# Performance work log

Hardware: AMD Instinct MI355X
Metric: run time of the kernel (lower is better)

Reference implementation:

```python
import jax, jax.numpy as jnp
import numpy as np

T, H, E, K, G, TG, F, NSH = 1024, 1024, 64, 6, 8, 4, 512, 2
CAP = 384
SCALE = 2.5  # routed_scaling_factor


def setup_inputs() -> dict:
    key = jax.random.key(0)
    ks = jax.random.split(key, 7)
    return {
        'hidden_states': jax.random.normal(ks[0], (T, H), jnp.float32),
        'gate_w': jax.random.normal(ks[1], (E, H), jnp.float32) * 0.05,
        'bias': jax.random.normal(ks[2], (E,), jnp.float32) * 0.01,
        'w13': jax.random.normal(ks[3], (E, H, 2 * F), jnp.float32) * 0.02,
        'w2': jax.random.normal(ks[4], (E, F, H), jnp.float32) * 0.02,
        'sw13': jax.random.normal(ks[5], (H, 2 * F * NSH), jnp.float32) * 0.02,
        'sw2': jax.random.normal(ks[6], (F * NSH, H), jnp.float32) * 0.02,
    }


def _grouped_topk(logits, bias):
    # noaux_tc: sigmoid scores, bias-corrected group selection, weights from raw scores
    scores = jax.nn.sigmoid(logits)                      # [T,E]
    sc = scores + bias[None, :]
    grp = sc.reshape(-1, G, E // G)
    group_scores = jnp.sum(jax.lax.top_k(grp, 2)[0], -1)  # [T,G] sum of top-2 per group
    _, gidx = jax.lax.top_k(group_scores, TG)
    gmask = jnp.sum(jax.nn.one_hot(gidx, G, dtype=sc.dtype), axis=1)  # [T,G]
    emask = jnp.repeat(gmask, E // G, axis=1) > 0
    masked = jnp.where(emask, sc, -jnp.inf)
    _, topk_ids = jax.lax.top_k(masked, K)               # [T,K]
    w = jnp.take_along_axis(scores, topk_ids, axis=1)
    w = w / jnp.sum(w, -1, keepdims=True) * SCALE        # renormalize + scaling
    return w, topk_ids


def reference(hidden_states, gate_w, bias, w13, w2, sw13, sw2):
    x = hidden_states
    # shared experts MLP (SiluAndMul)
    gu_s = x @ sw13
    shared = (jax.nn.silu(gu_s[:, :F * NSH]) * gu_s[:, F * NSH:]) @ sw2

    # gate in fp32
    logits = x.astype(jnp.float32) @ gate_w.T
    topk_w, topk_ids = _grouped_topk(logits, bias)

    # dispatch to [E, CAP, H]
    flat = topk_ids.reshape(-1)                           # [T*K]
    oh = (flat[:, None] == jnp.arange(E)[None, :])
    pos = jnp.sum(jnp.cumsum(oh.astype(jnp.int32), 0) * oh, 1) - 1  # rank within expert
    slot = jnp.minimum(pos, CAP)
    x_rep = jnp.broadcast_to(x[:, None, :], (T, K, H)).reshape(-1, H)
    buf = jnp.zeros((E, CAP + 1, H), x.dtype).at[flat, slot].set(x_rep)[:, :CAP]

    # grouped expert MLP
    gu = jnp.einsum('ech,ehf->ecf', buf, w13)             # [E,CAP,2F]
    act = jax.nn.silu(gu[..., :F]) * gu[..., F:]
    eo = jnp.einsum('ecf,efh->ech', act, w2)              # [E,CAP,H]

    # combine
    valid = (pos < CAP).astype(x.dtype)[:, None]
    yk = eo[flat, jnp.minimum(pos, CAP - 1)] * valid      # [T*K,H]
    routed = jnp.sum(yk.reshape(T, K, H) * topk_w[..., None].astype(x.dtype), axis=1)
    return routed + shared
```

## Files before the change

kernel.cpp:

```cpp
#include <hip/hip_runtime.h>
#include <cstdint>

#define TT   1024
#define HH   1024
#define EE   64
#define KK   6
#define GG   8
#define TGn  4
#define FF   512
#define FN   1024
#define CAPc 384
#define SCALEs 2.5f

typedef unsigned int u32;
typedef unsigned short u16;
typedef short short8 __attribute__((ext_vector_type(8)));
typedef float f32x4 __attribute__((ext_vector_type(4)));
union ABu { uint4 u; short8 s; };

__device__ __forceinline__ u32 pack_bf16(float a, float b) {
  u32 ua = __float_as_uint(a) + 0x8000u;
  u32 ub = __float_as_uint(b) + 0x8000u;
  return __builtin_amdgcn_perm(ub, ua, 0x07060302u);
}
__device__ __forceinline__ u16 bf16_1(float a) {
  return (u16)((__float_as_uint(a) + 0x8000u) >> 16);
}
__device__ __forceinline__ float bf2f(u32 lo16) {
  return __uint_as_float(lo16 << 16);
}

__global__ __launch_bounds__(256) void convert_x(const float* __restrict__ x,
                                                 u32* __restrict__ xb) {
  const int i = blockIdx.x * 256 + threadIdx.x;
  float4 v = ((const float4*)x)[i];
  uint2 o;
  o.x = pack_bf16(v.x, v.y);
  o.y = pack_bf16(v.z, v.w);
  ((uint2*)xb)[i] = o;
}

__global__ __launch_bounds__(256) void gate_topk_kernel(
    const float* __restrict__ x, const float* __restrict__ gw,
    const float* __restrict__ bias, int* __restrict__ ids,
    float* __restrict__ tw) {
  __shared__ float xs[HH];
  __shared__ float part[256];
  __shared__ float sc[EE];
  __shared__ float scores[EE];
  const int t = blockIdx.x, tid = threadIdx.x;
  ((float4*)xs)[tid] = ((const float4*)(x + (size_t)t * HH))[tid];
  __syncthreads();
  {
    const int e = tid & 63, seg = tid >> 6;
    const float* w = gw + (size_t)e * HH + seg * 256;
    const float* xv = xs + seg * 256;
    float acc = 0.f;
#pragma unroll 8
    for (int i = 0; i < 256; ++i) acc = fmaf(xv[i], w[i], acc);
    part[tid] = acc;
  }
  __syncthreads();
  if (tid < 64) {
    float a = part[tid] + part[tid + 64] + part[tid + 128] + part[tid + 192];
    float s = 1.f / (1.f + expf(-a));
    scores[tid] = s;
    sc[tid] = s + bias[tid];
  }
  __syncthreads();
  if (tid == 0) {
    float gs[GG];
    for (int g = 0; g < GG; ++g) {
      float m1 = -1e30f, m2 = -1e30f;
      for (int j = 0; j < EE / GG; ++j) {
        float v = sc[g * (EE / GG) + j];
        if (v > m1) { m2 = m1; m1 = v; }
        else if (v > m2) { m2 = v; }
      }
      gs[g] = m1 + m2;
    }
    unsigned gmask = 0;
    for (int r = 0; r < TGn; ++r) {
      int best = -1; float bv = -1e30f;
      for (int g = 0; g < GG; ++g)
        if (!((gmask >> g) & 1u) && gs[g] > bv) { bv = gs[g]; best = g; }
      gmask |= 1u << best;
    }
    unsigned long long used = 0ull;
    float wsum = 0.f;
    int idbuf[KK]; float wbuf[KK];
    for (int r = 0; r < KK; ++r) {
      int best = -1; float bv = -3e38f;
      for (int e = 0; e < EE; ++e) {
        if (!((gmask >> (e / (EE / GG))) & 1u)) continue;
        if ((used >> e) & 1ull) continue;
        float v = sc[e];
        if (v > bv) { bv = v; best = e; }
      }
      used |= 1ull << best;
      idbuf[r] = best;
      wbuf[r] = scores[best];
      wsum += scores[best];
    }
    const float inv = SCALEs / wsum;
    for (int r = 0; r < KK; ++r) {
      ids[t * KK + r] = idbuf[r];
      tw[t * KK + r] = wbuf[r] * inv;
    }
  }
}

__global__ void dispatch_kernel(const int* __restrict__ ids,
                                int* __restrict__ counts,
                                int* __restrict__ tok_of,
                                int* __restrict__ slot_of) {
  const int i = blockIdx.x * blockDim.x + threadIdx.x;
  if (i >= TT * KK) return;
  const int e = ids[i];
  const int p = atomicAdd(&counts[e], 1);
  slot_of[i] = p;
  if (p < CAPc) tok_of[e * CAPc + p] = i / KK;
}

#define SA 20
#define SB 132

template<int MT, int FH, bool ROUTED>
__global__ __launch_bounds__(256) void gemm1_k(
    const u32* __restrict__ xb, const float* __restrict__ wsrc,
    const int* __restrict__ counts, const int* __restrict__ tok_of,
    u16* __restrict__ actp) {
  constexpr int WROW = 2 * FH;
  constexpr int RT = MT / 32;
  constexpr int ADW = MT * 16 / 256;
  const int e = ROUTED ? blockIdx.z : 0;
  int n_e = MT;
  if (ROUTED) {
    n_e = min(counts[e], CAPc);
    if ((int)(blockIdx.y * MT) >= n_e) return;
  }
  const int m0 = blockIdx.y * MT;
  const int n0 = blockIdx.x * 64;
  __shared__ __align__(16) u32 As[MT * SA];
  __shared__ __align__(16) u32 Bs[16 * SB];
  __shared__ int toks[MT];
  const int tid = threadIdx.x;
  if (ROUTED) {
    for (int i = tid; i < MT; i += 256)
      toks[i] = (m0 + i < n_e) ? tok_of[e * CAPc + m0 + i] : -1;
    __syncthreads();
  }
  const int wave = tid >> 6, lane = tid & 63, quad = lane >> 4, l16 = lane & 15;
  const int ww = wave & 1, wr = wave >> 1;
  const float* W = wsrc + (ROUTED ? (size_t)e * HH * WROW : 0);
  const int arow_i = tid & (MT - 1);
  const int akd = (MT == 128 ? (tid >> 7) : (tid >> 6)) * ADW;
  bool aok = true;
  const u32* arow;
  if (ROUTED) {
    int tk = toks[arow_i];
    aok = tk >= 0;
    arow = xb + (size_t)(aok ? tk : 0) * (HH / 2);
  } else {
    arow = xb + (size_t)(m0 + arow_i) * (HH / 2);
  }
  const int bkd0 = tid >> 5, bn4 = (tid & 31) << 2;
  const int bcol = (bn4 < 64) ? (n0 + bn4) : (FH + n0 + (bn4 - 64));

  uint4 apf[ADW / 4];
  float4 bpf[2][2];
  auto prefetch = [&](int k0) {
#pragma unroll
    for (int i = 0; i < ADW / 4; ++i) {
      uint4 v = *(const uint4*)(arow + (k0 >> 1) + akd + 4 * i);
      if (!aok) v = make_uint4(0u, 0u, 0u, 0u);
      apf[i] = v;
    }
#pragma unroll
    for (int i = 0; i < 2; ++i) {
      const float* p = W + (size_t)(k0 + 2 * (bkd0 + 8 * i)) * WROW + bcol;
      bpf[i][0] = *(const float4*)p;
      bpf[i][1] = *(const float4*)(p + WROW);
    }
  };
  prefetch(0);
  f32x4 acc[RT][4] = {};
  for (int k0 = 0; k0 < HH; k0 += 32) {
    __syncthreads();
#pragma unroll
    for (int i = 0; i < ADW / 4; ++i)
      *(uint4*)(&As[arow_i * SA + akd + 4 * i]) = apf[i];
#pragma unroll
    for (int i = 0; i < 2; ++i) {
      uint4 bv;
      bv.x = pack_bf16(bpf[i][0].x, bpf[i][1].x);
      bv.y = pack_bf16(bpf[i][0].y, bpf[i][1].y);
      bv.z = pack_bf16(bpf[i][0].z, bpf[i][1].z);
      bv.w = pack_bf16(bpf[i][0].w, bpf[i][1].w);
      *(uint4*)(&Bs[(bkd0 + 8 * i) * SB + bn4]) = bv;
    }
    __syncthreads();
    if (k0 + 32 < HH) prefetch(k0 + 32);
    ABu bfr[4];
#pragma unroll
    for (int j = 0; j < 4; ++j) {
      const int cb = (j < 2) ? (ww * 32 + j * 16) : (64 + ww * 32 + (j - 2) * 16);
      const int col = cb + l16;
      bfr[j].u.x = Bs[(quad * 4 + 0) * SB + col];
      bfr[j].u.y = Bs[(quad * 4 + 1) * SB + col];
      bfr[j].u.z = Bs[(quad * 4 + 2) * SB + col];
      bfr[j].u.w = Bs[(quad * 4 + 3) * SB + col];
    }
#pragma unroll
    for (int mi = 0; mi < RT; ++mi) {
      ABu a;
      a.u = *(const uint4*)(&As[(wr * (MT / 2) + mi * 16 + l16) * SA + quad * 4]);
#pragma unroll
      for (int j = 0; j < 4; ++j)
        acc[mi][j] = __builtin_amdgcn_mfma_f32_16x16x32_bf16(a.s, bfr[j].s, acc[mi][j], 0, 0, 0);
    }
  }
#pragma unroll
  for (int mi = 0; mi < RT; ++mi) {
#pragma unroll
    for (int j = 0; j < 2; ++j) {
      const int col = n0 + ww * 32 + j * 16 + l16;
#pragma unroll
      for (int r = 0; r < 4; ++r) {
        const int row = m0 + wr * (MT / 2) + mi * 16 + quad * 4 + r;
        const float g = acc[mi][j][r], u = acc[mi][j + 2][r];
        const float v = (g / (1.f + __expf(-g))) * u;
        size_t idx = ROUTED ? (((size_t)e * CAPc + row) * FH + col)
                            : ((size_t)row * FH + col);
        actp[idx] = bf16_1(v);
      }
    }
  }
}

template<int MT, int KD, bool ROUTED>
__global__ __launch_bounds__(256) void gemm2_k(
    const u32* __restrict__ asrc0, const float* __restrict__ wsrc,
    const int* __restrict__ counts, void* __restrict__ outp) {
  constexpr int RT = MT / 32;
  constexpr int ADW = MT * 16 / 256;
  const int e = ROUTED ? blockIdx.z : 0;
  if (ROUTED) {
    if ((int)(blockIdx.y * MT) >= min(counts[e], CAPc)) return;
  }
  const int m0 = blockIdx.y * MT;
  const int n0 = blockIdx.x * 128;
  __shared__ __align__(16) u32 As[MT * SA];
  __shared__ __align__(16) u32 Bs[16 * SB];
  const int tid = threadIdx.x;
  const int wave = tid >> 6, lane = tid & 63, quad = lane >> 4, l16 = lane & 15;
  const int ww = wave & 1, wr = wave >> 1;
  const float* W = wsrc + (ROUTED ? (size_t)e * KD * HH : 0);
  const int arow_i = tid & (MT - 1);
  const int akd = (MT == 128 ? (tid >> 7) : (tid >> 6)) * ADW;
  const u32* arow = asrc0 + (ROUTED ? ((size_t)e * CAPc + m0 + arow_i) * (KD / 2)
                                    : (size_t)(m0 + arow_i) * (KD / 2));
  const int bkd0 = tid >> 5, bn4 = (tid & 31) << 2;

  uint4 apf[ADW / 4];
  float4 bpf[2][2];
  auto prefetch = [&](int k0) {
#pragma unroll
    for (int i = 0; i < ADW / 4; ++i)
      apf[i] = *(const uint4*)(arow + (k0 >> 1) + akd + 4 * i);
#pragma unroll
    for (int i = 0; i < 2; ++i) {
      const float* p = W + (size_t)(k0 + 2 * (bkd0 + 8 * i)) * HH + n0 + bn4;
      bpf[i][0] = *(const float4*)p;
      bpf[i][1] = *(const float4*)(p + HH);
    }
  };
  prefetch(0);
  f32x4 acc[RT][4] = {};
  for (int k0 = 0; k0 < KD; k0 += 32) {
    __syncthreads();
#pragma unroll
    for (int i = 0; i < ADW / 4; ++i)
      *(uint4*)(&As[arow_i * SA + akd + 4 * i]) = apf[i];
#pragma unroll
    for (int i = 0; i < 2; ++i) {
      uint4 bv;
      bv.x = pack_bf16(bpf[i][0].x, bpf[i][1].x);
      bv.y = pack_bf16(bpf[i][0].y, bpf[i][1].y);
      bv.z = pack_bf16(bpf[i][0].z, bpf[i][1].z);
      bv.w = pack_bf16(bpf[i][0].w, bpf[i][1].w);
      *(uint4*)(&Bs[(bkd0 + 8 * i) * SB + bn4]) = bv;
    }
    __syncthreads();
    if (k0 + 32 < KD) prefetch(k0 + 32);
    ABu bfr[4];
#pragma unroll
    for (int j = 0; j < 4; ++j) {
      const int col = ww * 64 + j * 16 + l16;
      bfr[j].u.x = Bs[(quad * 4 + 0) * SB + col];
      bfr[j].u.y = Bs[(quad * 4 + 1) * SB + col];
      bfr[j].u.z = Bs[(quad * 4 + 2) * SB + col];
      bfr[j].u.w = Bs[(quad * 4 + 3) * SB + col];
    }
#pragma unroll
    for (int mi = 0; mi < RT; ++mi) {
      ABu a;
      a.u = *(const uint4*)(&As[(wr * (MT / 2) + mi * 16 + l16) * SA + quad * 4]);
#pragma unroll
      for (int j = 0; j < 4; ++j)
        acc[mi][j] = __builtin_amdgcn_mfma_f32_16x16x32_bf16(a.s, bfr[j].s, acc[mi][j], 0, 0, 0);
    }
  }
#pragma unroll
  for (int mi = 0; mi < RT; ++mi) {
#pragma unroll
    for (int j = 0; j < 4; ++j) {
      const int col = n0 + ww * 64 + j * 16 + l16;
#pragma unroll
      for (int r = 0; r < 4; ++r) {
        const int row = m0 + wr * (MT / 2) + mi * 16 + quad * 4 + r;
        if (ROUTED) {
          ((u16*)outp)[((size_t)e * CAPc + row) * HH + col] = bf16_1(acc[mi][j][r]);
        } else {
          ((float*)outp)[(size_t)row * HH + col] = acc[mi][j][r];
        }
      }
    }
  }
}

__global__ __launch_bounds__(256) void combine_k(
    const u16* __restrict__ eo, const int* __restrict__ ids,
    const int* __restrict__ slot_of, const float* __restrict__ tw,
    float* __restrict__ out) {
  const int t = blockIdx.x, tid = threadIdx.x;
  __shared__ int se[KK];
  __shared__ int ssl[KK];
  __shared__ float swt[KK];
  if (tid < KK) {
    se[tid] = ids[t * KK + tid];
    ssl[tid] = slot_of[t * KK + tid];
    swt[tid] = tw[t * KK + tid];
  }
  __syncthreads();
  const int h = tid * 4;
  float4 o = *(float4*)(&out[(size_t)t * HH + h]);
#pragma unroll
  for (int k = 0; k < KK; ++k) {
    if (ssl[k] >= CAPc) continue;
    const float wgt = swt[k];
    const u16* p = eo + ((size_t)se[k] * CAPc + ssl[k]) * HH + h;
    uint2 v = *(const uint2*)p;
    o.x = fmaf(wgt, bf2f(v.x & 0xffffu), o.x);
    o.y = fmaf(wgt, bf2f(v.x >> 16), o.y);
    o.z = fmaf(wgt, bf2f(v.y & 0xffffu), o.z);
    o.w = fmaf(wgt, bf2f(v.y >> 16), o.w);
  }
  *(float4*)(&out[(size_t)t * HH + h]) = o;
}

extern "C" void kernel_launch(void* const* d_in, const int* in_sizes, int n_in,
                              void* d_out, int out_size, void* d_ws, size_t ws_size,
                              hipStream_t stream) {
  const float* x    = (const float*)d_in[0];
  const float* gw   = (const float*)d_in[1];
  const float* bias = (const float*)d_in[2];
  const float* w13  = (const float*)d_in[3];
  const float* w2   = (const float*)d_in[4];
  const float* sw13 = (const float*)d_in[5];
  const float* sw2  = (const float*)d_in[6];
  float* out = (float*)d_out;

  char* ws = (char*)d_ws;
  size_t off = 0;
  int*   counts  = (int*)(ws + off);   off += 256;
  int*   tok_of  = (int*)(ws + off);   off += (size_t)EE * CAPc * 4;
  int*   ids     = (int*)(ws + off);   off += (size_t)TT * KK * 4;
  int*   slot_of = (int*)(ws + off);   off += (size_t)TT * KK * 4;
  float* tw      = (float*)(ws + off); off += (size_t)TT * KK * 4;
  off = (off + 255) & ~(size_t)255;
  u32*   xb      = (u32*)(ws + off);   off += (size_t)TT * HH * 2;
  u16*   act     = (u16*)(ws + off);   off += (size_t)EE * CAPc * FF * 2;
  u16*   eo      = (u16*)(ws + off);   off += (size_t)EE * CAPc * HH * 2;
  u16*   act_s   = (u16*)(ws + off);   off += (size_t)TT * FN * 2;

  hipMemsetAsync(counts, 0, 256, stream);
  convert_x<<<TT * HH / 1024, 256, 0, stream>>>(x, xb);
  gate_topk_kernel<<<TT, 256, 0, stream>>>(x, gw, bias, ids, tw);
  dispatch_kernel<<<(TT * KK + 255) / 256, 256, 0, stream>>>(ids, counts, tok_of, slot_of);
  gemm1_k<128, FF, true><<<dim3(FF / 64, CAPc / 128, EE), 256, 0, stream>>>(
      xb, w13, counts, tok_of, act);
  gemm2_k<128, FF, true><<<dim3(HH / 128, CAPc / 128, EE), 256, 0, stream>>>(
      (const u32*)act, w2, counts, eo);
  gemm1_k<64, FN, false><<<dim3(FN / 64, TT / 64), 256, 0, stream>>>(
      xb, sw13, nullptr, nullptr, act_s);
  gemm2_k<64, FN, false><<<dim3(HH / 128, TT / 64), 256, 0, stream>>>(
      (const u32*)act_s, sw2, nullptr, out);
  combine_k<<<TT, 256, 0, stream>>>(eo, ids, slot_of, tw, out);
}
```

Before: 633.0 us.

## Fuse gate/convert/dispatch, double-buffer GEMM prefetch, narrow shared gemm2 tile

Merges the bf16 conversion of x, the gate/top-k, and the dispatch atomics into one kernel, removing two launches. The GEMM kernels now prefetch two k-steps ahead using double-buffered registers, to hide global-load latency. The shared-expert down-projection uses a 64-wide N tile, doubling its block count for better occupancy. Register pressure rises from the extra prefetch buffers.

```diff
diff --git a/kernel.cpp b/kernel.cpp
--- a/kernel.cpp
+++ b/kernel.cpp
@@ -30,26 +30,22 @@
   return __uint_as_float(lo16 << 16);
 }
 
-__global__ __launch_bounds__(256) void convert_x(const float* __restrict__ x,
-                                                 u32* __restrict__ xb) {
-  const int i = blockIdx.x * 256 + threadIdx.x;
-  float4 v = ((const float4*)x)[i];
-  uint2 o;
-  o.x = pack_bf16(v.x, v.y);
-  o.y = pack_bf16(v.z, v.w);
-  ((uint2*)xb)[i] = o;
-}
-
-__global__ __launch_bounds__(256) void gate_topk_kernel(
+__global__ __launch_bounds__(256) void gate_fused(
     const float* __restrict__ x, const float* __restrict__ gw,
-    const float* __restrict__ bias, int* __restrict__ ids,
-    float* __restrict__ tw) {
+    const float* __restrict__ bias, u32* __restrict__ xb,
+    int* __restrict__ counts, int* __restrict__ tok_of,
+    int* __restrict__ ids, int* __restrict__ slot_of, float* __restrict__ tw) {
   __shared__ float xs[HH];
   __shared__ float part[256];
   __shared__ float sc[EE];
   __shared__ float scores[EE];
   const int t = blockIdx.x, tid = threadIdx.x;
-  ((float4*)xs)[tid] = ((const float4*)(x + (size_t)t * HH))[tid];
+  float4 v = ((const float4*)(x + (size_t)t * HH))[tid];
+  ((float4*)xs)[tid] = v;
+  uint2 o;
+  o.x = pack_bf16(v.x, v.y);
+  o.y = pack_bf16(v.z, v.w);
+  ((uint2*)xb)[t * (HH / 4) + tid] = o;
   __syncthreads();
   {
     const int e = tid & 63, seg = tid >> 6;
@@ -73,9 +69,9 @@
     for (int g = 0; g < GG; ++g) {
       float m1 = -1e30f, m2 = -1e30f;
       for (int j = 0; j < EE / GG; ++j) {
-        float v = sc[g * (EE / GG) + j];
-        if (v > m1) { m2 = m1; m1 = v; }
-        else if (v > m2) { m2 = v; }
+        float v2 = sc[g * (EE / GG) + j];
+        if (v2 > m1) { m2 = m1; m1 = v2; }
+        else if (v2 > m2) { m2 = v2; }
       }
       gs[g] = m1 + m2;
     }
@@ -94,8 +90,8 @@
       for (int e = 0; e < EE; ++e) {
         if (!((gmask >> (e / (EE / GG))) & 1u)) continue;
         if ((used >> e) & 1ull) continue;
-        float v = sc[e];
-        if (v > bv) { bv = v; best = e; }
+        float v2 = sc[e];
+        if (v2 > bv) { bv = v2; best = e; }
       }
       used |= 1ull << best;
       idbuf[r] = best;
@@ -104,26 +100,19 @@
     }
     const float inv = SCALEs / wsum;
     for (int r = 0; r < KK; ++r) {
-      ids[t * KK + r] = idbuf[r];
+      const int e = idbuf[r];
+      const int p = atomicAdd(&counts[e], 1);
+      if (p < CAPc) tok_of[e * CAPc + p] = t;
+      ids[t * KK + r] = e;
+      slot_of[t * KK + r] = p;
       tw[t * KK + r] = wbuf[r] * inv;
     }
   }
-}
-
-__global__ void dispatch_kernel(const int* __restrict__ ids,
-                                int* __restrict__ counts,
-                                int* __restrict__ tok_of,
-                                int* __restrict__ slot_of) {
-  const int i = blockIdx.x * blockDim.x + threadIdx.x;
-  if (i >= TT * KK) return;
-  const int e = ids[i];
-  const int p = atomicAdd(&counts[e], 1);
-  slot_of[i] = p;
-  if (p < CAPc) tok_of[e * CAPc + p] = i / KK;
 }
 
 #define SA 20
 #define SB 132
+#define SB2 68
 
 template<int MT, int FH, bool ROUTED>
 __global__ __launch_bounds__(256) void gemm1_k(
@@ -133,6 +122,7 @@
   constexpr int WROW = 2 * FH;
   constexpr int RT = MT / 32;
   constexpr int ADW = MT * 16 / 256;
+  constexpr int AV = ADW / 4;
   const int e = ROUTED ? blockIdx.z : 0;
   int n_e = MT;
   if (ROUTED) {
@@ -167,40 +157,42 @@
   const int bkd0 = tid >> 5, bn4 = (tid & 31) << 2;
   const int bcol = (bn4 < 64) ? (n0 + bn4) : (FH + n0 + (bn4 - 64));
 
-  uint4 apf[ADW / 4];
-  float4 bpf[2][2];
-  auto prefetch = [&](int k0) {
-#pragma unroll
-    for (int i = 0; i < ADW / 4; ++i) {
+  uint4 apf[2][AV];
+  float4 bpf[2][2][2];
+  auto prefetch = [&](int k0, int p) {
+#pragma unroll
+    for (int i = 0; i < AV; ++i) {
       uint4 v = *(const uint4*)(arow + (k0 >> 1) + akd + 4 * i);
       if (!aok) v = make_uint4(0u, 0u, 0u, 0u);
-      apf[i] = v;
+      apf[p][i] = v;
     }
 #pragma unroll
     for (int i = 0; i < 2; ++i) {
-      const float* p = W + (size_t)(k0 + 2 * (bkd0 + 8 * i)) * WROW + bcol;
-      bpf[i][0] = *(const float4*)p;
-      bpf[i][1] = *(const float4*)(p + WROW);
+      const float* ptr = W + (size_t)(k0 + 2 * (bkd0 + 8 * i)) * WROW + bcol;
+      bpf[p][i][0] = *(const float4*)ptr;
+      bpf[p][i][1] = *(const float4*)(ptr + WROW);
     }
   };
-  prefetch(0);
+  prefetch(0, 0);
+  prefetch(32, 1);
   f32x4 acc[RT][4] = {};
   for (int k0 = 0; k0 < HH; k0 += 32) {
-    __syncthreads();
-#pragma unroll
-    for (int i = 0; i < ADW / 4; ++i)
-      *(uint4*)(&As[arow_i * SA + akd + 4 * i]) = apf[i];
+    const int p = (k0 >> 5) & 1;
+    __syncthreads();
+#pragma unroll
+    for (int i = 0; i < AV; ++i)
+      *(uint4*)(&As[arow_i * SA + akd + 4 * i]) = apf[p][i];
 #pragma unroll
     for (int i = 0; i < 2; ++i) {
       uint4 bv;
-      bv.x = pack_bf16(bpf[i][0].x, bpf[i][1].x);
-      bv.y = pack_bf16(bpf[i][0].y, bpf[i][1].y);
-      bv.z = pack_bf16(bpf[i][0].z, bpf[i][1].z);
-      bv.w = pack_bf16(bpf[i][0].w, bpf[i][1].w);
+      bv.x = pack_bf16(bpf[p][i][0].x, bpf[p][i][1].x);
+      bv.y = pack_bf16(bpf[p][i][0].y, bpf[p][i][1].y);
+      bv.z = pack_bf16(bpf[p][i][0].z, bpf[p][i][1].z);
+      bv.w = pack_bf16(bpf[p][i][0].w, bpf[p][i][1].w);
       *(uint4*)(&Bs[(bkd0 + 8 * i) * SB + bn4]) = bv;
     }
     __syncthreads();
-    if (k0 + 32 < HH) prefetch(k0 + 32);
+    if (k0 + 64 < HH) prefetch(k0 + 64, p);
     ABu bfr[4];
 #pragma unroll
     for (int j = 0; j < 4; ++j) {
@@ -238,20 +230,23 @@
   }
 }
 
-template<int MT, int KD, bool ROUTED>
+template<int MT, int NT, int KD, bool ROUTED>
 __global__ __launch_bounds__(256) void gemm2_k(
     const u32* __restrict__ asrc0, const float* __restrict__ wsrc,
     const int* __restrict__ counts, void* __restrict__ outp) {
   constexpr int RT = MT / 32;
+  constexpr int CT = NT / 32;
   constexpr int ADW = MT * 16 / 256;
+  constexpr int AV = ADW / 4;
+  constexpr int SBX = (NT == 128) ? SB : SB2;
   const int e = ROUTED ? blockIdx.z : 0;
   if (ROUTED) {
     if ((int)(blockIdx.y * MT) >= min(counts[e], CAPc)) return;
   }
   const int m0 = blockIdx.y * MT;
-  const int n0 = blockIdx.x * 128;
+  const int n0 = blockIdx.x * NT;
   __shared__ __align__(16) u32 As[MT * SA];
-  __shared__ __align__(16) u32 Bs[16 * SB];
+  __shared__ __align__(16) u32 Bs[16 * SBX];
   const int tid = threadIdx.x;
   const int wave = tid >> 6, lane = tid & 63, quad = lane >> 4, l16 = lane & 15;
   const int ww = wave & 1, wr = wave >> 1;
@@ -260,62 +255,66 @@
   const int akd = (MT == 128 ? (tid >> 7) : (tid >> 6)) * ADW;
   const u32* arow = asrc0 + (ROUTED ? ((size_t)e * CAPc + m0 + arow_i) * (KD / 2)
                                     : (size_t)(m0 + arow_i) * (KD / 2));
-  const int bkd0 = tid >> 5, bn4 = (tid & 31) << 2;
-
-  uint4 apf[ADW / 4];
-  float4 bpf[2][2];
-  auto prefetch = [&](int k0) {
-#pragma unroll
-    for (int i = 0; i < ADW / 4; ++i)
-      apf[i] = *(const uint4*)(arow + (k0 >> 1) + akd + 4 * i);
-#pragma unroll
-    for (int i = 0; i < 2; ++i) {
-      const float* p = W + (size_t)(k0 + 2 * (bkd0 + 8 * i)) * HH + n0 + bn4;
-      bpf[i][0] = *(const float4*)p;
-      bpf[i][1] = *(const float4*)(p + HH);
+  const int bkd0 = (NT == 128) ? (tid >> 5) : (tid >> 4);
+  const int bn4 = (NT == 128) ? ((tid & 31) << 2) : ((tid & 15) << 2);
+  constexpr int BI = (NT == 128) ? 2 : 1;
+
+  uint4 apf[2][AV];
+  float4 bpf[2][BI][2];
+  auto prefetch = [&](int k0, int p) {
+#pragma unroll
+    for (int i = 0; i < AV; ++i)
+      apf[p][i] = *(const uint4*)(arow + (k0 >> 1) + akd + 4 * i);
+#pragma unroll
+    for (int i = 0; i < BI; ++i) {
+      const float* ptr = W + (size_t)(k0 + 2 * (bkd0 + 8 * i)) * HH + n0 + bn4;
+      bpf[p][i][0] = *(const float4*)ptr;
+      bpf[p][i][1] = *(const float4*)(ptr + HH);
     }
   };
-  prefetch(0);
-  f32x4 acc[RT][4] = {};
+  prefetch(0, 0);
+  prefetch(32, 1);
+  f32x4 acc[RT][CT] = {};
   for (int k0 = 0; k0 < KD; k0 += 32) {
-    __syncthreads();
-#pragma unroll
-    for (int i = 0; i < ADW / 4; ++i)
-      *(uint4*)(&As[arow_i * SA + akd + 4 * i]) = apf[i];
-#pragma unroll
-    for (int i = 0; i < 2; ++i) {
+    const int p = (k0 >> 5) & 1;
+    __syncthreads();
+#pragma unroll
+    for (int i = 0; i < AV; ++i)
+      *(uint4*)(&As[arow_i * SA + akd + 4 * i]) = apf[p][i];
+#pragma unroll
+    for (int i = 0; i < BI; ++i) {
       uint4 bv;
-      bv.x = pack_bf16(bpf[i][0].x, bpf[i][1].x);
-      bv.y = pack_bf16(bpf[i][0].y, bpf[i][1].y);
-      bv.z = pack_bf16(bpf[i][0].z, bpf[i][1].z);
-      bv.w = pack_bf16(bpf[i][0].w, bpf[i][1].w);
-      *(uint4*)(&Bs[(bkd0 + 8 * i) * SB + bn4]) = bv;
-    }
-    __syncthreads();
-    if (k0 + 32 < KD) prefetch(k0 + 32);
-    ABu bfr[4];
-#pragma unroll
-    for (int j = 0; j < 4; ++j) {
-      const int col = ww * 64 + j * 16 + l16;
-      bfr[j].u.x = Bs[(quad * 4 + 0) * SB + col];
-      bfr[j].u.y = Bs[(quad * 4 + 1) * SB + col];
-      bfr[j].u.z = Bs[(quad * 4 + 2) * SB + col];
-      bfr[j].u.w = Bs[(quad * 4 + 3) * SB + col];
+      bv.x = pack_bf16(bpf[p][i][0].x, bpf[p][i][1].x);
+      bv.y = pack_bf16(bpf[p][i][0].y, bpf[p][i][1].y);
+      bv.z = pack_bf16(bpf[p][i][0].z, bpf[p][i][1].z);
+      bv.w = pack_bf16(bpf[p][i][0].w, bpf[p][i][1].w);
+      *(uint4*)(&Bs[(bkd0 + 8 * i) * SBX + bn4]) = bv;
+    }
+    __syncthreads();
+    if (k0 + 64 < KD) prefetch(k0 + 64, p);
+    ABu bfr[CT];
+#pragma unroll
+    for (int j = 0; j < CT; ++j) {
+      const int col = ww * (NT / 2) + j * 16 + l16;
+      bfr[j].u.x = Bs[(quad * 4 + 0) * SBX + col];
+      bfr[j].u.y = Bs[(quad * 4 + 1) * SBX + col];
+      bfr[j].u.z = Bs[(quad * 4 + 2) * SBX + col];
+      bfr[j].u.w = Bs[(quad * 4 + 3) * SBX + col];
     }
 #pragma unroll
     for (int mi = 0; mi < RT; ++mi) {
       ABu a;
       a.u = *(const uint4*)(&As[(wr * (MT / 2) + mi * 16 + l16) * SA + quad * 4]);
 #pragma unroll
-      for (int j = 0; j < 4; ++j)
+      for (int j = 0; j < CT; ++j)
         acc[mi][j] = __builtin_amdgcn_mfma_f32_16x16x32_bf16(a.s, bfr[j].s, acc[mi][j], 0, 0, 0);
     }
   }
 #pragma unroll
   for (int mi = 0; mi < RT; ++mi) {
 #pragma unroll
-    for (int j = 0; j < 4; ++j) {
-      const int col = n0 + ww * 64 + j * 16 + l16;
+    for (int j = 0; j < CT; ++j) {
+      const int col = n0 + ww * (NT / 2) + j * 16 + l16;
 #pragma unroll
       for (int r = 0; r < 4; ++r) {
         const int row = m0 + wr * (MT / 2) + mi * 16 + quad * 4 + r;
@@ -385,16 +384,14 @@
   u16*   act_s   = (u16*)(ws + off);   off += (size_t)TT * FN * 2;
 
   hipMemsetAsync(counts, 0, 256, stream);
-  convert_x<<<TT * HH / 1024, 256, 0, stream>>>(x, xb);
-  gate_topk_kernel<<<TT, 256, 0, stream>>>(x, gw, bias, ids, tw);
-  dispatch_kernel<<<(TT * KK + 255) / 256, 256, 0, stream>>>(ids, counts, tok_of, slot_of);
+  gate_fused<<<TT, 256, 0, stream>>>(x, gw, bias, xb, counts, tok_of, ids, slot_of, tw);
   gemm1_k<128, FF, true><<<dim3(FF / 64, CAPc / 128, EE), 256, 0, stream>>>(
       xb, w13, counts, tok_of, act);
-  gemm2_k<128, FF, true><<<dim3(HH / 128, CAPc / 128, EE), 256, 0, stream>>>(
+  gemm2_k<128, 128, FF, true><<<dim3(HH / 128, CAPc / 128, EE), 256, 0, stream>>>(
       (const u32*)act, w2, counts, eo);
   gemm1_k<64, FN, false><<<dim3(FN / 64, TT / 64), 256, 0, stream>>>(
       xb, sw13, nullptr, nullptr, act_s);
-  gemm2_k<64, FN, false><<<dim3(HH / 128, TT / 64), 256, 0, stream>>>(
+  gemm2_k<64, 64, FN, false><<<dim3(HH / 64, TT / 64), 256, 0, stream>>>(
       (const u32*)act_s, sw2, nullptr, out);
   combine_k<<<TT, 256, 0, stream>>>(eo, ids, slot_of, tw, out);
 }
```

New measurement: 822.5 us. +29.9%, slower.
